# Optimization experiments

Hardware: AMD Instinct MI355X
Metric: run time of the kernel (lower is better)

Reference implementation:

```python
import jax, jax.numpy as jnp
import numpy as np
import math

IN_C = 768
CA = 384
K1 = (3, 1, 1)
K2 = (1, 3, 3)
K3 = (3, 3, 3)


def _dwconv3d(x, w, b):
    # x: [B, Ca, T, H, W]; w: [Ca, 1, kt, kh, kw]; depthwise (groups = Ca)
    pads = [(k // 2, k // 2) for k in w.shape[2:]]
    y = jax.lax.conv_general_dilated(
        x, w, window_strides=(1, 1, 1), padding=pads,
        feature_group_count=x.shape[1],
        dimension_numbers=("NCDHW", "OIDHW", "NCDHW"))
    return y + b[None, :, None, None, None]


def setup_inputs() -> dict:
    key = jax.random.key(0)
    ks = jax.random.split(key, 12)
    s = 0.02
    x = jax.random.normal(ks[0], (128, 197, IN_C), dtype=jnp.float32)
    fc1_w = jax.random.normal(ks[1], (CA, IN_C), dtype=jnp.float32) * s
    fc1_b = jnp.zeros((CA,), dtype=jnp.float32)
    conv1_w = jax.random.normal(ks[2], (CA, 1) + K1, dtype=jnp.float32) * s
    conv1_b = jax.random.normal(ks[3], (CA,), dtype=jnp.float32) * s
    conv2_w = jax.random.normal(ks[4], (CA, 1) + K2, dtype=jnp.float32) * s
    conv2_b = jax.random.normal(ks[5], (CA,), dtype=jnp.float32) * s
    conv3_w = jax.random.normal(ks[6], (CA, 1) + K3, dtype=jnp.float32) * s
    conv3_b = jax.random.normal(ks[7], (CA,), dtype=jnp.float32) * s
    proj_w = jax.random.normal(ks[8], (CA, 1) + K1, dtype=jnp.float32) * s
    proj_b = jax.random.normal(ks[9], (CA,), dtype=jnp.float32) * s
    fc2_w = jax.random.normal(ks[10], (IN_C, CA), dtype=jnp.float32) * s
    fc2_b = jnp.zeros((IN_C,), dtype=jnp.float32)
    return {
        "x": x, "fc1_w": fc1_w, "fc1_b": fc1_b,
        "conv1_w": conv1_w, "conv1_b": conv1_b,
        "conv2_w": conv2_w, "conv2_b": conv2_b,
        "conv3_w": conv3_w, "conv3_b": conv3_b,
        "proj_w": proj_w, "proj_b": proj_b,
        "fc2_w": fc2_w, "fc2_b": fc2_b,
        "T": 16,
    }


def reference(x, fc1_w, fc1_b, conv1_w, conv1_b, conv2_w, conv2_b,
              conv3_w, conv3_b, proj_w, proj_b, fc2_w, fc2_b, T):
    BT, L, C = x.shape
    B = BT // T
    H = W = round(math.sqrt(L - 1))
    Ca = fc1_w.shape[0]
    x_id = x
    # drop CLS token, project down: [BT, L-1, Ca]
    h = jnp.einsum("blc,ac->bla", x[:, 1:, :], fc1_w) + fc1_b
    # [B, Ca, T, H, W]
    h = h.reshape(B, T, H, W, Ca).transpose(0, 4, 1, 2, 3)
    identity = h
    h = (_dwconv3d(h, conv1_w, conv1_b)
         + _dwconv3d(h, conv2_w, conv2_b)
         + _dwconv3d(h, conv3_w, conv3_b)) / 3.0
    h = h + identity
    h = h + _dwconv3d(h, proj_w, proj_b)
    # back to tokens: [BT, L-1, Ca]
    h = h.transpose(0, 2, 3, 4, 1).reshape(BT, L - 1, Ca)
    h = jnp.einsum("bla,ca->blc", h, fc2_w) + fc2_b
    return x_id.at[:, 1:, :].add(h)
```

## Files before the change

### kernel.cpp

```cpp
#include <hip/hip_runtime.h>
#include <cstdint>

typedef __bf16 bf16_t;
typedef __bf16 bf16x8 __attribute__((ext_vector_type(8)));
typedef float f32x4 __attribute__((ext_vector_type(4)));

#define BT_   128
#define LTOK  197
#define CIN   768
#define CA_   384
#define TT    16
#define HH    14
#define NTOK  25088

__device__ __forceinline__ void gl_lds16(const void* g, void* l) {
  __builtin_amdgcn_global_load_lds(
      (const __attribute__((address_space(1))) unsigned int*)g,
      (__attribute__((address_space(3))) unsigned int*)l,
      16, 0, 0);
}

__global__ void prep_weights_kernel(
    const float* __restrict__ c1w, const float* __restrict__ c1b,
    const float* __restrict__ c2w, const float* __restrict__ c2b,
    const float* __restrict__ c3w, const float* __restrict__ c3b,
    const float* __restrict__ projw,
    bf16_t* __restrict__ Wtb,
    float* __restrict__ beff,
    float* __restrict__ pwt) {
  int a = blockIdx.x * blockDim.x + threadIdx.x;
  if (a >= CA_) return;
  for (int dt = 0; dt < 3; dt++)
    for (int dh = 0; dh < 3; dh++)
      for (int dw = 0; dw < 3; dw++) {
        float v = c3w[a*27 + dt*9 + dh*3 + dw];
        if (dh == 1 && dw == 1) v += c1w[a*3 + dt];
        if (dt == 1)            v += c2w[a*9 + dh*3 + dw];
        v *= (1.0f/3.0f);
        if (dt == 1 && dh == 1 && dw == 1) v += 1.0f;
        Wtb[((dt*3+dh)*3+dw)*CA_ + a] = (bf16_t)v;
      }
  beff[a] = (c1b[a] + c2b[a] + c3b[a]) * (1.0f/3.0f);
  pwt[0*CA_ + a] = projw[a*3 + 0];
  pwt[1*CA_ + a] = projw[a*3 + 1];
  pwt[2*CA_ + a] = projw[a*3 + 2];
}

__global__ void convert_w_kernel(const float* __restrict__ fc1w,
                                 const float* __restrict__ fc2w,
                                 const float* __restrict__ x,
                                 float* __restrict__ out,
                                 bf16_t* __restrict__ W1,
                                 bf16_t* __restrict__ W2) {
  int i = blockIdx.x * blockDim.x + threadIdx.x;
  if (i < CA_*CIN) { W1[i] = (bf16_t)fc1w[i]; return; }
  i -= CA_*CIN;
  if (i < CIN*CA_) { W2[i] = (bf16_t)fc2w[i]; return; }
  i -= CIN*CA_;
  if (i < BT_*CIN) {
    int bt = i / CIN, c = i % CIN;
    size_t off = (size_t)bt * LTOK * CIN + c;
    out[off] = x[off];
  }
}

__global__ __launch_bounds__(256) void gemm1_kernel(
    const float* __restrict__ x, const bf16_t* __restrict__ W1,
    const float* __restrict__ fc1b, bf16_t* __restrict__ H0) {
  __shared__ bf16_t Alds[128*32];
  __shared__ bf16_t Blds[128*32];
  const int tid  = threadIdx.x;
  const int lane = tid & 63;
  const int wave = tid >> 6;
  const int bm = blockIdx.x, bn = blockIdx.y;

  const int arow  = tid >> 1;
  const int kbase = (tid & 1) * 16;
  const int tok   = bm*128 + arow;
  const int bt    = tok / 196;
  const float* xrow = x + (size_t)(tok + bt + 1) * CIN + kbase;
  bf16_t* alds_dst = &Alds[arow*32 + kbase];

  const bf16_t* bsrc0 = W1 + (size_t)(bn*128 + (tid>>2))*CIN + (tid&3)*8;
  const bf16_t* bsrc1 = bsrc0 + (size_t)64*CIN;
  bf16_t* blds0 = &Blds[tid*8];
  bf16_t* blds1 = &Blds[(tid+256)*8];

  const int quad = lane >> 4;
  const int r16  = lane & 15;
  const int wm = (wave >> 1) * 64;
  const int wn = (wave & 1) * 64;

  f32x4 acc[4][4] = {};

  for (int k0 = 0; k0 < CIN; k0 += 32) {
    gl_lds16(bsrc0 + k0, blds0);
    gl_lds16(bsrc1 + k0, blds1);
    const float4* xp = (const float4*)(xrow + k0);
    float4 f0 = xp[0], f1 = xp[1], f2 = xp[2], f3 = xp[3];
    bf16x8 p0, p1;
    p0[0]=(bf16_t)f0.x; p0[1]=(bf16_t)f0.y; p0[2]=(bf16_t)f0.z; p0[3]=(bf16_t)f0.w;
    p0[4]=(bf16_t)f1.x; p0[5]=(bf16_t)f1.y; p0[6]=(bf16_t)f1.z; p0[7]=(bf16_t)f1.w;
    p1[0]=(bf16_t)f2.x; p1[1]=(bf16_t)f2.y; p1[2]=(bf16_t)f2.z; p1[3]=(bf16_t)f2.w;
    p1[4]=(bf16_t)f3.x; p1[5]=(bf16_t)f3.y; p1[6]=(bf16_t)f3.z; p1[7]=(bf16_t)f3.w;
    *(bf16x8*)alds_dst       = p0;
    *(bf16x8*)(alds_dst + 8) = p1;
    __syncthreads();
    bf16x8 af[4], bfr[4];
    #pragma unroll
    for (int mt = 0; mt < 4; mt++)
      af[mt] = *(const bf16x8*)&Alds[(wm + mt*16 + r16)*32 + quad*8];
    #pragma unroll
    for (int nt = 0; nt < 4; nt++)
      bfr[nt] = *(const bf16x8*)&Blds[(wn + nt*16 + r16)*32 + quad*8];
    #pragma unroll
    for (int mt = 0; mt < 4; mt++)
      #pragma unroll
      for (int nt = 0; nt < 4; nt++)
        acc[mt][nt] = __builtin_amdgcn_mfma_f32_16x16x32_bf16(af[mt], bfr[nt], acc[mt][nt], 0, 0, 0);
    __syncthreads();
  }

  #pragma unroll
  for (int nt = 0; nt < 4; nt++) {
    const int col = bn*128 + wn + nt*16 + r16;
    const float bias = fc1b[col];
    #pragma unroll
    for (int mt = 0; mt < 4; mt++) {
      const int row0 = bm*128 + wm + mt*16 + quad*4;
      #pragma unroll
      for (int rg = 0; rg < 4; rg++)
        H0[(size_t)(row0 + rg)*CA_ + col] = (bf16_t)(acc[mt][nt][rg] + bias);
    }
  }
}

__global__ __launch_bounds__(192) void conv_kernel(
    const bf16_t* __restrict__ H0,
    const bf16_t* __restrict__ Wtb,
    const float* __restrict__ beff,
    const float* __restrict__ pwt,
    const float* __restrict__ pb,
    bf16_t* __restrict__ Z) {
  __shared__ bf16_t Wlds[27*CA_];
  __shared__ float  ybuf[2][2][CA_];

  const int tid = threadIdx.x;
  {
    const uint4* src = (const uint4*)Wtb;
    uint4* dst = (uint4*)Wlds;
    #pragma unroll
    for (int i = 0; i < 7; i++) {
      int idx = tid + i*192;
      if (idx < 27*CA_/8) dst[idx] = src[idx];
    }
  }

  const int blk  = blockIdx.x;
  const int b    = blk & 7;
  const int pair = blk >> 3;
  const int cg   = tid % 48;
  const int ct   = tid / 48;
  const int col  = ct >> 1;
  const int th   = ct & 1;
  const int hw   = pair*2 + col;
  const int h    = hw / HH, w = hw % HH;
  const int c0   = cg * 8;
  const int t0   = th * 8;

  float y[8][8];
  {
    f32x4 bv0 = *(const f32x4*)(beff + c0);
    f32x4 bv1 = *(const f32x4*)(beff + c0 + 4);
    #pragma unroll
    for (int i = 0; i < 8; i++) {
      #pragma unroll
      for (int c = 0; c < 4; c++) { y[i][c] = bv0[c]; y[i][c+4] = bv1[c]; }
    }
  }

  __syncthreads();

  const size_t rowstride = (size_t)196*CA_;
  const bf16_t* base_t0 = H0 + ((size_t)(b*TT + t0)*196)*CA_ + c0;
  const int tau_e_off = th ? -1 : 8;

  for (int j = 0; j < 9; j++) {
    const int dh = j / 3, dw = j - dh*3;
    const int h2 = h + dh - 1, w2 = w + dw - 1;
    const bool ok = ((unsigned)h2 < HH) && ((unsigned)w2 < HH);
    const int sp = ok ? (h2*HH + w2) : hw;
    const float m = ok ? 1.0f : 0.0f;

    const bf16x8 wv0 = *(const bf16x8*)&Wlds[(0*9+j)*CA_ + c0];
    const bf16x8 wv1 = *(const bf16x8*)&Wlds[(1*9+j)*CA_ + c0];
    const bf16x8 wv2 = *(const bf16x8*)&Wlds[(2*9+j)*CA_ + c0];
    float mw0[8], mw1[8], mw2[8];
    #pragma unroll
    for (int c = 0; c < 8; c++) {
      mw0[c] = m * (float)wv0[c];
      mw1[c] = m * (float)wv1[c];
      mw2[c] = m * (float)wv2[c];
    }

    const bf16_t* tp = base_t0 + (size_t)sp*CA_;
    bf16x8 gv[8];
    #pragma unroll
    for (int i = 0; i < 8; i++)
      gv[i] = *(const bf16x8*)(tp + (ptrdiff_t)i*(ptrdiff_t)rowstride);
    const bf16x8 ge = *(const bf16x8*)(tp + (ptrdiff_t)tau_e_off*(ptrdiff_t)rowstride);

    #pragma unroll
    for (int i = 0; i < 8; i++) {
      float gf[8];
      #pragma unroll
      for (int c = 0; c < 8; c++) gf[c] = (float)gv[i][c];
      #pragma unroll
      for (int c = 0; c < 8; c++) y[i][c] += gf[c]*mw1[c];
      if (i > 0) {
        #pragma unroll
        for (int c = 0; c < 8; c++) y[i-1][c] += gf[c]*mw2[c];
      }
      if (i < 7) {
        #pragma unroll
        for (int c = 0; c < 8; c++) y[i+1][c] += gf[c]*mw0[c];
      }
    }
    {
      float gf[8];
      #pragma unroll
      for (int c = 0; c < 8; c++) gf[c] = (float)ge[c];
      if (th) {
        #pragma unroll
        for (int c = 0; c < 8; c++) y[0][c] += gf[c]*mw0[c];
      } else {
        #pragma unroll
        for (int c = 0; c < 8; c++) y[7][c] += gf[c]*mw2[c];
      }
    }
  }

  #pragma unroll
  for (int c = 0; c < 8; c++) ybuf[col][th][c0+c] = th ? y[0][c] : y[7][c];
  __syncthreads();
  float yedge[8];
  #pragma unroll
  for (int c = 0; c < 8; c++) yedge[c] = ybuf[col][1-th][c0+c];

  float p0[8], p1[8], p2[8], pbv[8];
  {
    f32x4 a0 = *(const f32x4*)(pwt + 0*CA_ + c0), a1 = *(const f32x4*)(pwt + 0*CA_ + c0 + 4);
    f32x4 b0 = *(const f32x4*)(pwt + 1*CA_ + c0), b1 = *(const f32x4*)(pwt + 1*CA_ + c0 + 4);
    f32x4 d0 = *(const f32x4*)(pwt + 2*CA_ + c0), d1 = *(const f32x4*)(pwt + 2*CA_ + c0 + 4);
    f32x4 e0 = *(const f32x4*)(pb + c0),          e1 = *(const f32x4*)(pb + c0 + 4);
    #pragma unroll
    for (int c = 0; c < 4; c++) {
      p0[c]=a0[c]; p0[c+4]=a1[c];
      p1[c]=b0[c]; p1[c+4]=b1[c];
      p2[c]=d0[c]; p2[c+4]=d1[c];
      pbv[c]=e0[c]; pbv[c+4]=e1[c];
    }
  }

  bf16_t* zbase = Z + ((size_t)(b*TT + t0)*196 + hw)*CA_ + c0;
  #pragma unroll
  for (int i = 0; i < 8; i++) {
    bf16x8 zo;
    #pragma unroll
    for (int c = 0; c < 8; c++) {
      const float ym = (i > 0) ? y[i-1][c] : (th ? yedge[c] : 0.f);
      const float yp = (i < 7) ? y[i+1][c] : (th ? 0.f : yedge[c]);
      const float z  = y[i][c] + pbv[c] + p0[c]*ym + p1[c]*y[i][c] + p2[c]*yp;
      zo[c] = (bf16_t)z;
    }
    *(bf16x8*)(zbase + (size_t)i*rowstride) = zo;
  }
}

__global__ __launch_bounds__(256) void gemm2_kernel(
    const bf16_t* __restrict__ Z, const bf16_t* __restrict__ W2,
    const float* __restrict__ fc2b, const float* __restrict__ x,
    float* __restrict__ out) {
  __shared__ bf16_t Alds[128*32];
  __shared__ bf16_t Blds[128*32];
  const int tid  = threadIdx.x;
  const int lane = tid & 63;
  const int wave = tid >> 6;
  const int bm = blockIdx.x, bn = blockIdx.y;

  const bf16_t* asrc0 = Z  + (size_t)(bm*128 + (tid>>2))*CA_ + (tid&3)*8;
  const bf16_t* asrc1 = asrc0 + (size_t)64*CA_;
  const bf16_t* bsrc0 = W2 + (size_t)(bn*128 + (tid>>2))*CA_ + (tid&3)*8;
  const bf16_t* bsrc1 = bsrc0 + (size_t)64*CA_;
  bf16_t* alds0 = &Alds[tid*8];
  bf16_t* alds1 = &Alds[(tid+256)*8];
  bf16_t* blds0 = &Blds[tid*8];
  bf16_t* blds1 = &Blds[(tid+256)*8];

  const int quad = lane >> 4;
  const int r16  = lane & 15;
  const int wm = (wave >> 1) * 64;
  const int wn = (wave & 1) * 64;

  f32x4 acc[4][4] = {};

  for (int k0 = 0; k0 < CA_; k0 += 32) {
    gl_lds16(asrc0 + k0, alds0);
    gl_lds16(asrc1 + k0, alds1);
    gl_lds16(bsrc0 + k0, blds0);
    gl_lds16(bsrc1 + k0, blds1);
    __syncthreads();
    bf16x8 af[4], bfr[4];
    #pragma unroll
    for (int mt = 0; mt < 4; mt++)
      af[mt] = *(const bf16x8*)&Alds[(wm + mt*16 + r16)*32 + quad*8];
    #pragma unroll
    for (int nt = 0; nt < 4; nt++)
      bfr[nt] = *(const bf16x8*)&Blds[(wn + nt*16 + r16)*32 + quad*8];
    #pragma unroll
    for (int mt = 0; mt < 4; mt++)
      #pragma unroll
      for (int nt = 0; nt < 4; nt++)
        acc[mt][nt] = __builtin_amdgcn_mfma_f32_16x16x32_bf16(af[mt], bfr[nt], acc[mt][nt], 0, 0, 0);
    __syncthreads();
  }

  #pragma unroll
  for (int nt = 0; nt < 4; nt++) {
    const int col = bn*128 + wn + nt*16 + r16;
    const float bias = fc2b[col];
    #pragma unroll
    for (int mt = 0; mt < 4; mt++) {
      #pragma unroll
      for (int rg = 0; rg < 4; rg++) {
        const int tok = bm*128 + wm + mt*16 + quad*4 + rg;
        const int bt  = tok / 196;
        const size_t o = (size_t)(tok + bt + 1)*CIN + col;
        out[o] = x[o] + acc[mt][nt][rg] + bias;
      }
    }
  }
}

extern "C" void kernel_launch(void* const* d_in, const int* in_sizes, int n_in,
                              void* d_out, int out_size, void* d_ws, size_t ws_size,
                              hipStream_t stream) {
  (void)in_sizes; (void)n_in; (void)out_size; (void)ws_size;
  const float* x    = (const float*)d_in[0];
  const float* fc1w = (const float*)d_in[1];
  const float* fc1b = (const float*)d_in[2];
  const float* c1w  = (const float*)d_in[3];
  const float* c1b  = (const float*)d_in[4];
  const float* c2w  = (const float*)d_in[5];
  const float* c2b  = (const float*)d_in[6];
  const float* c3w  = (const float*)d_in[7];
  const float* c3b  = (const float*)d_in[8];
  const float* pw   = (const float*)d_in[9];
  const float* pb   = (const float*)d_in[10];
  const float* fc2w = (const float*)d_in[11];
  const float* fc2b = (const float*)d_in[12];
  float* out = (float*)d_out;

  char* ws = (char*)d_ws;
  bf16_t* W1   = (bf16_t*)(ws);
  bf16_t* W2   = (bf16_t*)(ws + 589824);
  bf16_t* Wtb  = (bf16_t*)(ws + 1179648);
  float*  beff = (float*) (ws + 1200384);
  float*  pwt  = (float*) (ws + 1201920);
  bf16_t* H0   = (bf16_t*)(ws + 1206528);
  bf16_t* Z    = (bf16_t*)(ws + 20474112);

  prep_weights_kernel<<<dim3(2), dim3(192), 0, stream>>>(
      c1w, c1b, c2w, c2b, c3w, c3b, pw, Wtb, beff, pwt);
  convert_w_kernel<<<dim3(2688), dim3(256), 0, stream>>>(fc1w, fc2w, x, out, W1, W2);
  gemm1_kernel<<<dim3(196, 3), dim3(256), 0, stream>>>(x, W1, fc1b, H0);
  conv_kernel<<<dim3(784), dim3(192), 0, stream>>>(H0, Wtb, beff, pwt, pb, Z);
  gemm2_kernel<<<dim3(196, 6), dim3(256), 0, stream>>>(Z, W2, fc2b, x, out);
}
```

Measured before the change: 262.1 us.

## Double-buffer LDS tiles in both GEMM kernels to overlap loads with MFMA

```diff
diff --git a/kernel.cpp b/kernel.cpp
--- a/kernel.cpp
+++ b/kernel.cpp
@@ -67,8 +67,8 @@
 __global__ __launch_bounds__(256) void gemm1_kernel(
     const float* __restrict__ x, const bf16_t* __restrict__ W1,
     const float* __restrict__ fc1b, bf16_t* __restrict__ H0) {
-  __shared__ bf16_t Alds[128*32];
-  __shared__ bf16_t Blds[128*32];
+  __shared__ bf16_t Alds[2][128*32];
+  __shared__ bf16_t Blds[2][128*32];
   const int tid  = threadIdx.x;
   const int lane = tid & 63;
   const int wave = tid >> 6;
@@ -79,12 +79,12 @@
   const int tok   = bm*128 + arow;
   const int bt    = tok / 196;
   const float* xrow = x + (size_t)(tok + bt + 1) * CIN + kbase;
-  bf16_t* alds_dst = &Alds[arow*32 + kbase];
+  const int aoff = arow*32 + kbase;
 
   const bf16_t* bsrc0 = W1 + (size_t)(bn*128 + (tid>>2))*CIN + (tid&3)*8;
   const bf16_t* bsrc1 = bsrc0 + (size_t)64*CIN;
-  bf16_t* blds0 = &Blds[tid*8];
-  bf16_t* blds1 = &Blds[(tid+256)*8];
+  const int boff0 = tid*8;
+  const int boff1 = (tid+256)*8;
 
   const int quad = lane >> 4;
   const int r16  = lane & 15;
@@ -93,32 +93,57 @@
 
   f32x4 acc[4][4] = {};
 
-  for (int k0 = 0; k0 < CIN; k0 += 32) {
-    gl_lds16(bsrc0 + k0, blds0);
-    gl_lds16(bsrc1 + k0, blds1);
-    const float4* xp = (const float4*)(xrow + k0);
+  {
+    const float4* xp = (const float4*)xrow;
     float4 f0 = xp[0], f1 = xp[1], f2 = xp[2], f3 = xp[3];
+    gl_lds16(bsrc0, &Blds[0][boff0]);
+    gl_lds16(bsrc1, &Blds[0][boff1]);
     bf16x8 p0, p1;
     p0[0]=(bf16_t)f0.x; p0[1]=(bf16_t)f0.y; p0[2]=(bf16_t)f0.z; p0[3]=(bf16_t)f0.w;
     p0[4]=(bf16_t)f1.x; p0[5]=(bf16_t)f1.y; p0[6]=(bf16_t)f1.z; p0[7]=(bf16_t)f1.w;
     p1[0]=(bf16_t)f2.x; p1[1]=(bf16_t)f2.y; p1[2]=(bf16_t)f2.z; p1[3]=(bf16_t)f2.w;
     p1[4]=(bf16_t)f3.x; p1[5]=(bf16_t)f3.y; p1[6]=(bf16_t)f3.z; p1[7]=(bf16_t)f3.w;
-    *(bf16x8*)alds_dst       = p0;
-    *(bf16x8*)(alds_dst + 8) = p1;
-    __syncthreads();
+    *(bf16x8*)&Alds[0][aoff]     = p0;
+    *(bf16x8*)&Alds[0][aoff + 8] = p1;
+  }
+  __syncthreads();
+
+  int cur = 0;
+  for (int k0 = 0; k0 < CIN; k0 += 32) {
+    const int kn = k0 + 32;
+    const bool more = (kn < CIN);
+    float4 f0, f1, f2, f3;
+    if (more) {
+      const float4* xp = (const float4*)(xrow + kn);
+      f0 = xp[0]; f1 = xp[1]; f2 = xp[2]; f3 = xp[3];
+      gl_lds16(bsrc0 + kn, &Blds[cur^1][boff0]);
+      gl_lds16(bsrc1 + kn, &Blds[cur^1][boff1]);
+    }
+
     bf16x8 af[4], bfr[4];
     #pragma unroll
     for (int mt = 0; mt < 4; mt++)
-      af[mt] = *(const bf16x8*)&Alds[(wm + mt*16 + r16)*32 + quad*8];
+      af[mt] = *(const bf16x8*)&Alds[cur][(wm + mt*16 + r16)*32 + quad*8];
     #pragma unroll
     for (int nt = 0; nt < 4; nt++)
-      bfr[nt] = *(const bf16x8*)&Blds[(wn + nt*16 + r16)*32 + quad*8];
+      bfr[nt] = *(const bf16x8*)&Blds[cur][(wn + nt*16 + r16)*32 + quad*8];
     #pragma unroll
     for (int mt = 0; mt < 4; mt++)
       #pragma unroll
       for (int nt = 0; nt < 4; nt++)
         acc[mt][nt] = __builtin_amdgcn_mfma_f32_16x16x32_bf16(af[mt], bfr[nt], acc[mt][nt], 0, 0, 0);
+
+    if (more) {
+      bf16x8 p0, p1;
+      p0[0]=(bf16_t)f0.x; p0[1]=(bf16_t)f0.y; p0[2]=(bf16_t)f0.z; p0[3]=(bf16_t)f0.w;
+      p0[4]=(bf16_t)f1.x; p0[5]=(bf16_t)f1.y; p0[6]=(bf16_t)f1.z; p0[7]=(bf16_t)f1.w;
+      p1[0]=(bf16_t)f2.x; p1[1]=(bf16_t)f2.y; p1[2]=(bf16_t)f2.z; p1[3]=(bf16_t)f2.w;
+      p1[4]=(bf16_t)f3.x; p1[5]=(bf16_t)f3.y; p1[6]=(bf16_t)f3.z; p1[7]=(bf16_t)f3.w;
+      *(bf16x8*)&Alds[cur^1][aoff]     = p0;
+      *(bf16x8*)&Alds[cur^1][aoff + 8] = p1;
+    }
     __syncthreads();
+    cur ^= 1;
   }
 
   #pragma unroll
@@ -281,8 +306,8 @@
     const bf16_t* __restrict__ Z, const bf16_t* __restrict__ W2,
     const float* __restrict__ fc2b, const float* __restrict__ x,
     float* __restrict__ out) {
-  __shared__ bf16_t Alds[128*32];
-  __shared__ bf16_t Blds[128*32];
+  __shared__ bf16_t Alds[2][128*32];
+  __shared__ bf16_t Blds[2][128*32];
   const int tid  = threadIdx.x;
   const int lane = tid & 63;
   const int wave = tid >> 6;
@@ -292,10 +317,8 @@
   const bf16_t* asrc1 = asrc0 + (size_t)64*CA_;
   const bf16_t* bsrc0 = W2 + (size_t)(bn*128 + (tid>>2))*CA_ + (tid&3)*8;
   const bf16_t* bsrc1 = bsrc0 + (size_t)64*CA_;
-  bf16_t* alds0 = &Alds[tid*8];
-  bf16_t* alds1 = &Alds[(tid+256)*8];
-  bf16_t* blds0 = &Blds[tid*8];
-  bf16_t* blds1 = &Blds[(tid+256)*8];
+  const int aoff0 = tid*8;
+  const int aoff1 = (tid+256)*8;
 
   const int quad = lane >> 4;
   const int r16  = lane & 15;
@@ -304,25 +327,35 @@
 
   f32x4 acc[4][4] = {};
 
+  gl_lds16(asrc0, &Alds[0][aoff0]);
+  gl_lds16(asrc1, &Alds[0][aoff1]);
+  gl_lds16(bsrc0, &Blds[0][aoff0]);
+  gl_lds16(bsrc1, &Blds[0][aoff1]);
+  __syncthreads();
+
+  int cur = 0;
   for (int k0 = 0; k0 < CA_; k0 += 32) {
-    gl_lds16(asrc0 + k0, alds0);
-    gl_lds16(asrc1 + k0, alds1);
-    gl_lds16(bsrc0 + k0, blds0);
-    gl_lds16(bsrc1 + k0, blds1);
-    __syncthreads();
+    const int kn = k0 + 32;
+    if (kn < CA_) {
+      gl_lds16(asrc0 + kn, &Alds[cur^1][aoff0]);
+      gl_lds16(asrc1 + kn, &Alds[cur^1][aoff1]);
+      gl_lds16(bsrc0 + kn, &Blds[cur^1][aoff0]);
+      gl_lds16(bsrc1 + kn, &Blds[cur^1][aoff1]);
+    }
     bf16x8 af[4], bfr[4];
     #pragma unroll
     for (int mt = 0; mt < 4; mt++)
-      af[mt] = *(const bf16x8*)&Alds[(wm + mt*16 + r16)*32 + quad*8];
+      af[mt] = *(const bf16x8*)&Alds[cur][(wm + mt*16 + r16)*32 + quad*8];
     #pragma unroll
     for (int nt = 0; nt < 4; nt++)
-      bfr[nt] = *(const bf16x8*)&Blds[(wn + nt*16 + r16)*32 + quad*8];
+      bfr[nt] = *(const bf16x8*)&Blds[cur][(wn + nt*16 + r16)*32 + quad*8];
     #pragma unroll
     for (int mt = 0; mt < 4; mt++)
       #pragma unroll
       for (int nt = 0; nt < 4; nt++)
         acc[mt][nt] = __builtin_amdgcn_mfma_f32_16x16x32_bf16(af[mt], bfr[nt], acc[mt][nt], 0, 0, 0);
     __syncthreads();
+    cur ^= 1;
   }
 
   #pragma unroll
```

Result: no change. 262.4 us (+0.1%).

## Triple-buffer LDS pipelines in both GEMMs with 64x192 tiles

Applied to the files above, without the earlier changes.

```diff
diff --git a/kernel.cpp b/kernel.cpp
--- a/kernel.cpp
+++ b/kernel.cpp
@@ -19,6 +19,10 @@
       (__attribute__((address_space(3))) unsigned int*)l,
       16, 0, 0);
 }
+
+#define SBAR() do { __builtin_amdgcn_sched_barrier(0); \
+                    __builtin_amdgcn_s_barrier(); \
+                    __builtin_amdgcn_sched_barrier(0); } while (0)
 
 __global__ void prep_weights_kernel(
     const float* __restrict__ c1w, const float* __restrict__ c1b,
@@ -67,72 +71,103 @@
 __global__ __launch_bounds__(256) void gemm1_kernel(
     const float* __restrict__ x, const bf16_t* __restrict__ W1,
     const float* __restrict__ fc1b, bf16_t* __restrict__ H0) {
-  __shared__ bf16_t Alds[128*32];
-  __shared__ bf16_t Blds[128*32];
+  __shared__ bf16_t Alds[3][2048];
+  __shared__ bf16_t Blds[3][6144];
   const int tid  = threadIdx.x;
   const int lane = tid & 63;
   const int wave = tid >> 6;
   const int bm = blockIdx.x, bn = blockIdx.y;
 
-  const int arow  = tid >> 1;
-  const int kbase = (tid & 1) * 16;
-  const int tok   = bm*128 + arow;
-  const int bt    = tok / 196;
-  const float* xrow = x + (size_t)(tok + bt + 1) * CIN + kbase;
-  bf16_t* alds_dst = &Alds[arow*32 + kbase];
-
-  const bf16_t* bsrc0 = W1 + (size_t)(bn*128 + (tid>>2))*CIN + (tid&3)*8;
-  const bf16_t* bsrc1 = bsrc0 + (size_t)64*CIN;
-  bf16_t* blds0 = &Blds[tid*8];
-  bf16_t* blds1 = &Blds[(tid+256)*8];
+  const int arow = tid >> 2;
+  const int tok  = bm*64 + arow;
+  const int bt   = tok / 196;
+  const float* xsrc = x + (size_t)(tok + bt + 1)*CIN + (tid & 3)*8;
+  const bf16_t* bsrc = W1 + (size_t)(bn*192 + arow)*CIN + (tid & 3)*8;
 
   const int quad = lane >> 4;
   const int r16  = lane & 15;
-  const int wm = (wave >> 1) * 64;
-  const int wn = (wave & 1) * 64;
-
-  f32x4 acc[4][4] = {};
-
-  for (int k0 = 0; k0 < CIN; k0 += 32) {
-    gl_lds16(bsrc0 + k0, blds0);
-    gl_lds16(bsrc1 + k0, blds1);
-    const float4* xp = (const float4*)(xrow + k0);
-    float4 f0 = xp[0], f1 = xp[1], f2 = xp[2], f3 = xp[3];
-    bf16x8 p0, p1;
-    p0[0]=(bf16_t)f0.x; p0[1]=(bf16_t)f0.y; p0[2]=(bf16_t)f0.z; p0[3]=(bf16_t)f0.w;
-    p0[4]=(bf16_t)f1.x; p0[5]=(bf16_t)f1.y; p0[6]=(bf16_t)f1.z; p0[7]=(bf16_t)f1.w;
-    p1[0]=(bf16_t)f2.x; p1[1]=(bf16_t)f2.y; p1[2]=(bf16_t)f2.z; p1[3]=(bf16_t)f2.w;
-    p1[4]=(bf16_t)f3.x; p1[5]=(bf16_t)f3.y; p1[6]=(bf16_t)f3.z; p1[7]=(bf16_t)f3.w;
-    *(bf16x8*)alds_dst       = p0;
-    *(bf16x8*)(alds_dst + 8) = p1;
-    __syncthreads();
-    bf16x8 af[4], bfr[4];
-    #pragma unroll
-    for (int mt = 0; mt < 4; mt++)
-      af[mt] = *(const bf16x8*)&Alds[(wm + mt*16 + r16)*32 + quad*8];
-    #pragma unroll
-    for (int nt = 0; nt < 4; nt++)
-      bfr[nt] = *(const bf16x8*)&Blds[(wn + nt*16 + r16)*32 + quad*8];
-    #pragma unroll
-    for (int mt = 0; mt < 4; mt++)
-      #pragma unroll
-      for (int nt = 0; nt < 4; nt++)
-        acc[mt][nt] = __builtin_amdgcn_mfma_f32_16x16x32_bf16(af[mt], bfr[nt], acc[mt][nt], 0, 0, 0);
-    __syncthreads();
-  }
+  const int wn   = wave * 48;
+
+  f32x4 acc[4][3] = {};
+  float4 fa, fb;
+  float4 ca, cb;
+
+#define G1_LDF(K) do { const float4* xp_ = (const float4*)(xsrc + (K)); \
+                       fa = xp_[0]; fb = xp_[1]; } while (0)
+#define G1_GLB(B, K) do { const bf16_t* s_ = bsrc + (K); \
+    bf16_t* d_ = &Blds[B][0] + tid*8; \
+    gl_lds16(s_,                   d_); \
+    gl_lds16(s_ +  64*(size_t)CIN, d_ + 2048); \
+    gl_lds16(s_ + 128*(size_t)CIN, d_ + 4096); } while (0)
+#define G1_CVT(B) do { bf16x8 p_; \
+    p_[0]=(bf16_t)ca.x; p_[1]=(bf16_t)ca.y; p_[2]=(bf16_t)ca.z; p_[3]=(bf16_t)ca.w; \
+    p_[4]=(bf16_t)cb.x; p_[5]=(bf16_t)cb.y; p_[6]=(bf16_t)cb.z; p_[7]=(bf16_t)cb.w; \
+    *(bf16x8*)(&Alds[B][0] + tid*8) = p_; \
+    ca = fa; cb = fb; } while (0)
+#define G1_MMA(B) do { bf16x8 af_[4], bf_[3]; \
+    _Pragma("unroll") \
+    for (int mt = 0; mt < 4; mt++) \
+      af_[mt] = *(const bf16x8*)(&Alds[B][0] + (mt*16 + r16)*32 + quad*8); \
+    _Pragma("unroll") \
+    for (int nt = 0; nt < 3; nt++) \
+      bf_[nt] = *(const bf16x8*)(&Blds[B][0] + (wn + nt*16 + r16)*32 + quad*8); \
+    _Pragma("unroll") \
+    for (int mt = 0; mt < 4; mt++) \
+      _Pragma("unroll") \
+      for (int nt = 0; nt < 3; nt++) \
+        acc[mt][nt] = __builtin_amdgcn_mfma_f32_16x16x32_bf16(af_[mt], bf_[nt], acc[mt][nt], 0, 0, 0); \
+  } while (0)
+
+  { const float4* xp_ = (const float4*)xsrc; ca = xp_[0]; cb = xp_[1]; }
+  G1_GLB(0, 0);
+  G1_LDF(32);
+  G1_GLB(1, 32);
+  G1_CVT(0);
+  asm volatile("s_waitcnt vmcnt(5) lgkmcnt(0)" ::: "memory");
+  SBAR();
+
+  #pragma unroll 1
+  for (int ii = 0; ii < 7; ii++) {
+    #pragma unroll
+    for (int j = 0; j < 3; j++) {
+      const int i  = ii*3 + j;
+      const int kc = i*32;
+      G1_LDF(kc + 64);
+      G1_GLB((j + 2) % 3, kc + 64);
+      G1_MMA(j);
+      G1_CVT((j + 1) % 3);
+      asm volatile("s_waitcnt vmcnt(5) lgkmcnt(0)" ::: "memory");
+      SBAR();
+    }
+  }
+  G1_LDF(23*32);
+  G1_GLB(2, 23*32);
+  G1_MMA(0);
+  G1_CVT(1);
+  asm volatile("s_waitcnt vmcnt(5) lgkmcnt(0)" ::: "memory");
+  SBAR();
+  G1_MMA(1);
+  G1_CVT(2);
+  asm volatile("s_waitcnt vmcnt(0) lgkmcnt(0)" ::: "memory");
+  SBAR();
+  G1_MMA(2);
 
   #pragma unroll
-  for (int nt = 0; nt < 4; nt++) {
-    const int col = bn*128 + wn + nt*16 + r16;
+  for (int nt = 0; nt < 3; nt++) {
+    const int col = bn*192 + wn + nt*16 + r16;
     const float bias = fc1b[col];
     #pragma unroll
     for (int mt = 0; mt < 4; mt++) {
-      const int row0 = bm*128 + wm + mt*16 + quad*4;
+      const int row0 = bm*64 + mt*16 + quad*4;
       #pragma unroll
       for (int rg = 0; rg < 4; rg++)
         H0[(size_t)(row0 + rg)*CA_ + col] = (bf16_t)(acc[mt][nt][rg] + bias);
     }
   }
+#undef G1_LDF
+#undef G1_GLB
+#undef G1_CVT
+#undef G1_MMA
 }
 
 __global__ __launch_bounds__(192) void conv_kernel(
@@ -281,65 +316,86 @@
     const bf16_t* __restrict__ Z, const bf16_t* __restrict__ W2,
     const float* __restrict__ fc2b, const float* __restrict__ x,
     float* __restrict__ out) {
-  __shared__ bf16_t Alds[128*32];
-  __shared__ bf16_t Blds[128*32];
+  __shared__ bf16_t Alds[3][2048];
+  __shared__ bf16_t Blds[3][6144];
   const int tid  = threadIdx.x;
   const int lane = tid & 63;
   const int wave = tid >> 6;
   const int bm = blockIdx.x, bn = blockIdx.y;
 
-  const bf16_t* asrc0 = Z  + (size_t)(bm*128 + (tid>>2))*CA_ + (tid&3)*8;
-  const bf16_t* asrc1 = asrc0 + (size_t)64*CA_;
-  const bf16_t* bsrc0 = W2 + (size_t)(bn*128 + (tid>>2))*CA_ + (tid&3)*8;
-  const bf16_t* bsrc1 = bsrc0 + (size_t)64*CA_;
-  bf16_t* alds0 = &Alds[tid*8];
-  bf16_t* alds1 = &Alds[(tid+256)*8];
-  bf16_t* blds0 = &Blds[tid*8];
-  bf16_t* blds1 = &Blds[(tid+256)*8];
+  const int arow = tid >> 2;
+  const bf16_t* asrc = Z  + (size_t)(bm*64  + arow)*CA_ + (tid & 3)*8;
+  const bf16_t* bsrc = W2 + (size_t)(bn*192 + arow)*CA_ + (tid & 3)*8;
 
   const int quad = lane >> 4;
   const int r16  = lane & 15;
-  const int wm = (wave >> 1) * 64;
-  const int wn = (wave & 1) * 64;
-
-  f32x4 acc[4][4] = {};
-
-  for (int k0 = 0; k0 < CA_; k0 += 32) {
-    gl_lds16(asrc0 + k0, alds0);
-    gl_lds16(asrc1 + k0, alds1);
-    gl_lds16(bsrc0 + k0, blds0);
-    gl_lds16(bsrc1 + k0, blds1);
-    __syncthreads();
-    bf16x8 af[4], bfr[4];
-    #pragma unroll
-    for (int mt = 0; mt < 4; mt++)
-      af[mt] = *(const bf16x8*)&Alds[(wm + mt*16 + r16)*32 + quad*8];
-    #pragma unroll
-    for (int nt = 0; nt < 4; nt++)
-      bfr[nt] = *(const bf16x8*)&Blds[(wn + nt*16 + r16)*32 + quad*8];
-    #pragma unroll
-    for (int mt = 0; mt < 4; mt++)
-      #pragma unroll
-      for (int nt = 0; nt < 4; nt++)
-        acc[mt][nt] = __builtin_amdgcn_mfma_f32_16x16x32_bf16(af[mt], bfr[nt], acc[mt][nt], 0, 0, 0);
-    __syncthreads();
-  }
+  const int wn   = wave * 48;
+
+  f32x4 acc[4][3] = {};
+
+#define G2_GL(B, K) do { \
+    gl_lds16(asrc + (K), &Alds[B][0] + tid*8); \
+    const bf16_t* s_ = bsrc + (K); \
+    bf16_t* d_ = &Blds[B][0] + tid*8; \
+    gl_lds16(s_,                   d_); \
+    gl_lds16(s_ +  64*(size_t)CA_, d_ + 2048); \
+    gl_lds16(s_ + 128*(size_t)CA_, d_ + 4096); } while (0)
+#define G2_MMA(B) do { bf16x8 af_[4], bf_[3]; \
+    _Pragma("unroll") \
+    for (int mt = 0; mt < 4; mt++) \
+      af_[mt] = *(const bf16x8*)(&Alds[B][0] + (mt*16 + r16)*32 + quad*8); \
+    _Pragma("unroll") \
+    for (int nt = 0; nt < 3; nt++) \
+      bf_[nt] = *(const bf16x8*)(&Blds[B][0] + (wn + nt*16 + r16)*32 + quad*8); \
+    _Pragma("unroll") \
+    for (int mt = 0; mt < 4; mt++) \
+      _Pragma("unroll") \
+      for (int nt = 0; nt < 3; nt++) \
+        acc[mt][nt] = __builtin_amdgcn_mfma_f32_16x16x32_bf16(af_[mt], bf_[nt], acc[mt][nt], 0, 0, 0); \
+  } while (0)
+
+  G2_GL(0, 0);
+  G2_GL(1, 32);
+  asm volatile("s_waitcnt vmcnt(4)" ::: "memory");
+  SBAR();
+
+  #pragma unroll 1
+  for (int ii = 0; ii < 3; ii++) {
+    #pragma unroll
+    for (int j = 0; j < 3; j++) {
+      const int i = ii*3 + j;
+      G2_GL((j + 2) % 3, i*32 + 64);
+      G2_MMA(j);
+      asm volatile("s_waitcnt vmcnt(4)" ::: "memory");
+      SBAR();
+    }
+  }
+  G2_GL(2, 11*32);
+  G2_MMA(0);
+  asm volatile("s_waitcnt vmcnt(4)" ::: "memory");
+  SBAR();
+  G2_MMA(1);
+  asm volatile("s_waitcnt vmcnt(0)" ::: "memory");
+  SBAR();
+  G2_MMA(2);
 
   #pragma unroll
-  for (int nt = 0; nt < 4; nt++) {
-    const int col = bn*128 + wn + nt*16 + r16;
+  for (int nt = 0; nt < 3; nt++) {
+    const int col = bn*192 + wn + nt*16 + r16;
     const float bias = fc2b[col];
     #pragma unroll
     for (int mt = 0; mt < 4; mt++) {
       #pragma unroll
       for (int rg = 0; rg < 4; rg++) {
-        const int tok = bm*128 + wm + mt*16 + quad*4 + rg;
+        const int tok = bm*64 + mt*16 + quad*4 + rg;
         const int bt  = tok / 196;
         const size_t o = (size_t)(tok + bt + 1)*CIN + col;
         out[o] = x[o] + acc[mt][nt][rg] + bias;
       }
     }
   }
+#undef G2_GL
+#undef G2_MMA
 }
 
 extern "C" void kernel_launch(void* const* d_in, const int* in_sizes, int n_in,
@@ -373,7 +429,7 @@
   prep_weights_kernel<<<dim3(2), dim3(192), 0, stream>>>(
       c1w, c1b, c2w, c2b, c3w, c3b, pw, Wtb, beff, pwt);
   convert_w_kernel<<<dim3(2688), dim3(256), 0, stream>>>(fc1w, fc2w, x, out, W1, W2);
-  gemm1_kernel<<<dim3(196, 3), dim3(256), 0, stream>>>(x, W1, fc1b, H0);
+  gemm1_kernel<<<dim3(392, 2), dim3(256), 0, stream>>>(x, W1, fc1b, H0);
   conv_kernel<<<dim3(784), dim3(192), 0, stream>>>(H0, Wtb, beff, pwt, pb, Z);
-  gemm2_kernel<<<dim3(196, 6), dim3(256), 0, stream>>>(Z, W2, fc2b, x, out);
-}
+  gemm2_kernel<<<dim3(392, 4), dim3(256), 0, stream>>>(Z, W2, fc2b, x, out);
+}
```

Result: slower. 283.2 us (+8.1%).

## Pre-swizzle GEMM weights into MFMA fragment layout and drop LDS staging

Applied to the files above, without the earlier changes.

```diff
diff --git a/kernel.cpp b/kernel.cpp
--- a/kernel.cpp
+++ b/kernel.cpp
@@ -12,13 +12,6 @@
 #define TT    16
 #define HH    14
 #define NTOK  25088
-
-__device__ __forceinline__ void gl_lds16(const void* g, void* l) {
-  __builtin_amdgcn_global_load_lds(
-      (const __attribute__((address_space(1))) unsigned int*)g,
-      (__attribute__((address_space(3))) unsigned int*)l,
-      16, 0, 0);
-}
 
 __global__ void prep_weights_kernel(
     const float* __restrict__ c1w, const float* __restrict__ c1b,
@@ -50,12 +43,26 @@
                                  const float* __restrict__ fc2w,
                                  const float* __restrict__ x,
                                  float* __restrict__ out,
-                                 bf16_t* __restrict__ W1,
-                                 bf16_t* __restrict__ W2) {
+                                 bf16_t* __restrict__ W1f,
+                                 bf16_t* __restrict__ W2f) {
   int i = blockIdx.x * blockDim.x + threadIdx.x;
-  if (i < CA_*CIN) { W1[i] = (bf16_t)fc1w[i]; return; }
+  if (i < CA_*CIN) {
+    int f = i >> 9, t = i & 511, l = t >> 3, j = t & 7;
+    int ch = f / 24, cb = f % 24;
+    int col = cb*16 + (l & 15);
+    int k   = ch*32 + (l >> 4)*8 + j;
+    W1f[i] = (bf16_t)fc1w[col*CIN + k];
+    return;
+  }
   i -= CA_*CIN;
-  if (i < CIN*CA_) { W2[i] = (bf16_t)fc2w[i]; return; }
+  if (i < CIN*CA_) {
+    int f = i >> 9, t = i & 511, l = t >> 3, j = t & 7;
+    int ch = f / 48, cb = f % 48;
+    int col = cb*16 + (l & 15);
+    int k   = ch*32 + (l >> 4)*8 + j;
+    W2f[i] = (bf16_t)fc2w[col*CA_ + k];
+    return;
+  }
   i -= CIN*CA_;
   if (i < BT_*CIN) {
     int bt = i / CIN, c = i % CIN;
@@ -64,70 +71,53 @@
   }
 }
 
-__global__ __launch_bounds__(256) void gemm1_kernel(
-    const float* __restrict__ x, const bf16_t* __restrict__ W1,
+__global__ __launch_bounds__(64) void gemm1_kernel(
+    const float* __restrict__ x, const bf16_t* __restrict__ W1f,
     const float* __restrict__ fc1b, bf16_t* __restrict__ H0) {
-  __shared__ bf16_t Alds[128*32];
-  __shared__ bf16_t Blds[128*32];
-  const int tid  = threadIdx.x;
-  const int lane = tid & 63;
-  const int wave = tid >> 6;
-  const int bm = blockIdx.x, bn = blockIdx.y;
-
-  const int arow  = tid >> 1;
-  const int kbase = (tid & 1) * 16;
-  const int tok   = bm*128 + arow;
-  const int bt    = tok / 196;
-  const float* xrow = x + (size_t)(tok + bt + 1) * CIN + kbase;
-  bf16_t* alds_dst = &Alds[arow*32 + kbase];
-
-  const bf16_t* bsrc0 = W1 + (size_t)(bn*128 + (tid>>2))*CIN + (tid&3)*8;
-  const bf16_t* bsrc1 = bsrc0 + (size_t)64*CIN;
-  bf16_t* blds0 = &Blds[tid*8];
-  bf16_t* blds1 = &Blds[(tid+256)*8];
-
-  const int quad = lane >> 4;
-  const int r16  = lane & 15;
-  const int wm = (wave >> 1) * 64;
-  const int wn = (wave & 1) * 64;
-
-  f32x4 acc[4][4] = {};
-
-  for (int k0 = 0; k0 < CIN; k0 += 32) {
-    gl_lds16(bsrc0 + k0, blds0);
-    gl_lds16(bsrc1 + k0, blds1);
-    const float4* xp = (const float4*)(xrow + k0);
-    float4 f0 = xp[0], f1 = xp[1], f2 = xp[2], f3 = xp[3];
-    bf16x8 p0, p1;
-    p0[0]=(bf16_t)f0.x; p0[1]=(bf16_t)f0.y; p0[2]=(bf16_t)f0.z; p0[3]=(bf16_t)f0.w;
-    p0[4]=(bf16_t)f1.x; p0[5]=(bf16_t)f1.y; p0[6]=(bf16_t)f1.z; p0[7]=(bf16_t)f1.w;
-    p1[0]=(bf16_t)f2.x; p1[1]=(bf16_t)f2.y; p1[2]=(bf16_t)f2.z; p1[3]=(bf16_t)f2.w;
-    p1[4]=(bf16_t)f3.x; p1[5]=(bf16_t)f3.y; p1[6]=(bf16_t)f3.z; p1[7]=(bf16_t)f3.w;
-    *(bf16x8*)alds_dst       = p0;
-    *(bf16x8*)(alds_dst + 8) = p1;
-    __syncthreads();
-    bf16x8 af[4], bfr[4];
+  const int lane = threadIdx.x;
+  const int wg = blockIdx.x;
+  const int bm = blockIdx.y;
+  const int quad = lane >> 4, r16 = lane & 15;
+  const int wn = wg * 96;
+
+  const float* xa[4];
+  #pragma unroll
+  for (int mt = 0; mt < 4; mt++) {
+    int tok = bm*64 + mt*16 + r16;
+    int bt = tok / 196;
+    xa[mt] = x + (size_t)(tok + bt + 1)*CIN + quad*8;
+  }
+  const bf16_t* wb = W1f + (size_t)(wg*6)*512 + lane*8;
+
+  f32x4 acc[4][6] = {};
+  #pragma unroll
+  for (int i = 0; i < 24; i++) {
+    bf16x8 bfr[6];
+    #pragma unroll
+    for (int nt = 0; nt < 6; nt++)
+      bfr[nt] = *(const bf16x8*)(wb + (size_t)(i*24 + nt)*512);
+    bf16x8 af[4];
+    #pragma unroll
+    for (int mt = 0; mt < 4; mt++) {
+      const float4* p = (const float4*)(xa[mt] + i*32);
+      float4 u = p[0], v = p[1];
+      af[mt][0]=(bf16_t)u.x; af[mt][1]=(bf16_t)u.y; af[mt][2]=(bf16_t)u.z; af[mt][3]=(bf16_t)u.w;
+      af[mt][4]=(bf16_t)v.x; af[mt][5]=(bf16_t)v.y; af[mt][6]=(bf16_t)v.z; af[mt][7]=(bf16_t)v.w;
+    }
     #pragma unroll
     for (int mt = 0; mt < 4; mt++)
-      af[mt] = *(const bf16x8*)&Alds[(wm + mt*16 + r16)*32 + quad*8];
-    #pragma unroll
-    for (int nt = 0; nt < 4; nt++)
-      bfr[nt] = *(const bf16x8*)&Blds[(wn + nt*16 + r16)*32 + quad*8];
-    #pragma unroll
-    for (int mt = 0; mt < 4; mt++)
-      #pragma unroll
-      for (int nt = 0; nt < 4; nt++)
+      #pragma unroll
+      for (int nt = 0; nt < 6; nt++)
         acc[mt][nt] = __builtin_amdgcn_mfma_f32_16x16x32_bf16(af[mt], bfr[nt], acc[mt][nt], 0, 0, 0);
-    __syncthreads();
-  }
-
-  #pragma unroll
-  for (int nt = 0; nt < 4; nt++) {
-    const int col = bn*128 + wn + nt*16 + r16;
+  }
+
+  #pragma unroll
+  for (int nt = 0; nt < 6; nt++) {
+    const int col = wn + nt*16 + r16;
     const float bias = fc1b[col];
     #pragma unroll
     for (int mt = 0; mt < 4; mt++) {
-      const int row0 = bm*128 + wm + mt*16 + quad*4;
+      const int row0 = bm*64 + mt*16 + quad*4;
       #pragma unroll
       for (int rg = 0; rg < 4; rg++)
         H0[(size_t)(row0 + rg)*CA_ + col] = (bf16_t)(acc[mt][nt][rg] + bias);
@@ -277,66 +267,54 @@
   }
 }
 
-__global__ __launch_bounds__(256) void gemm2_kernel(
-    const bf16_t* __restrict__ Z, const bf16_t* __restrict__ W2,
+__global__ __launch_bounds__(64) void gemm2_kernel(
+    const bf16_t* __restrict__ Z, const bf16_t* __restrict__ W2f,
     const float* __restrict__ fc2b, const float* __restrict__ x,
     float* __restrict__ out) {
-  __shared__ bf16_t Alds[128*32];
-  __shared__ bf16_t Blds[128*32];
-  const int tid  = threadIdx.x;
-  const int lane = tid & 63;
-  const int wave = tid >> 6;
-  const int bm = blockIdx.x, bn = blockIdx.y;
-
-  const bf16_t* asrc0 = Z  + (size_t)(bm*128 + (tid>>2))*CA_ + (tid&3)*8;
-  const bf16_t* asrc1 = asrc0 + (size_t)64*CA_;
-  const bf16_t* bsrc0 = W2 + (size_t)(bn*128 + (tid>>2))*CA_ + (tid&3)*8;
-  const bf16_t* bsrc1 = bsrc0 + (size_t)64*CA_;
-  bf16_t* alds0 = &Alds[tid*8];
-  bf16_t* alds1 = &Alds[(tid+256)*8];
-  bf16_t* blds0 = &Blds[tid*8];
-  bf16_t* blds1 = &Blds[(tid+256)*8];
-
-  const int quad = lane >> 4;
-  const int r16  = lane & 15;
-  const int wm = (wave >> 1) * 64;
-  const int wn = (wave & 1) * 64;
-
-  f32x4 acc[4][4] = {};
-
-  for (int k0 = 0; k0 < CA_; k0 += 32) {
-    gl_lds16(asrc0 + k0, alds0);
-    gl_lds16(asrc1 + k0, alds1);
-    gl_lds16(bsrc0 + k0, blds0);
-    gl_lds16(bsrc1 + k0, blds1);
-    __syncthreads();
-    bf16x8 af[4], bfr[4];
+  const int lane = threadIdx.x;
+  const int wg = blockIdx.x;
+  const int bm = blockIdx.y;
+  const int quad = lane >> 4, r16 = lane & 15;
+  const int wn = wg * 96;
+
+  const bf16_t* za[4];
+  #pragma unroll
+  for (int mt = 0; mt < 4; mt++) {
+    int tok = bm*64 + mt*16 + r16;
+    za[mt] = Z + (size_t)tok*CA_ + quad*8;
+  }
+  const bf16_t* wb = W2f + (size_t)(wg*6)*512 + lane*8;
+
+  f32x4 acc[4][6] = {};
+  #pragma unroll
+  for (int i = 0; i < 12; i++) {
+    bf16x8 bfr[6];
+    #pragma unroll
+    for (int nt = 0; nt < 6; nt++)
+      bfr[nt] = *(const bf16x8*)(wb + (size_t)(i*48 + nt)*512);
+    bf16x8 af[4];
     #pragma unroll
     for (int mt = 0; mt < 4; mt++)
-      af[mt] = *(const bf16x8*)&Alds[(wm + mt*16 + r16)*32 + quad*8];
-    #pragma unroll
-    for (int nt = 0; nt < 4; nt++)
-      bfr[nt] = *(const bf16x8*)&Blds[(wn + nt*16 + r16)*32 + quad*8];
+      af[mt] = *(const bf16x8*)(za[mt] + i*32);
     #pragma unroll
     for (int mt = 0; mt < 4; mt++)
       #pragma unroll
-      for (int nt = 0; nt < 4; nt++)
+      for (int nt = 0; nt < 6; nt++)
         acc[mt][nt] = __builtin_amdgcn_mfma_f32_16x16x32_bf16(af[mt], bfr[nt], acc[mt][nt], 0, 0, 0);
-    __syncthreads();
-  }
-
-  #pragma unroll
-  for (int nt = 0; nt < 4; nt++) {
-    const int col = bn*128 + wn + nt*16 + r16;
-    const float bias = fc2b[col];
-    #pragma unroll
-    for (int mt = 0; mt < 4; mt++) {
-      #pragma unroll
-      for (int rg = 0; rg < 4; rg++) {
-        const int tok = bm*128 + wm + mt*16 + quad*4 + rg;
-        const int bt  = tok / 196;
-        const size_t o = (size_t)(tok + bt + 1)*CIN + col;
-        out[o] = x[o] + acc[mt][nt][rg] + bias;
+  }
+
+  #pragma unroll
+  for (int mt = 0; mt < 4; mt++) {
+    #pragma unroll
+    for (int rg = 0; rg < 4; rg++) {
+      const int tok = bm*64 + mt*16 + quad*4 + rg;
+      const int bt = tok / 196;
+      const size_t rowo = (size_t)(tok + bt + 1)*CIN;
+      #pragma unroll
+      for (int nt = 0; nt < 6; nt++) {
+        const int col = wn + nt*16 + r16;
+        const size_t o = rowo + col;
+        out[o] = x[o] + acc[mt][nt][rg] + fc2b[col];
       }
     }
   }
@@ -362,18 +340,18 @@
   float* out = (float*)d_out;
 
   char* ws = (char*)d_ws;
-  bf16_t* W1   = (bf16_t*)(ws);
-  bf16_t* W2   = (bf16_t*)(ws + 589824);
-  bf16_t* Wtb  = (bf16_t*)(ws + 1179648);
-  float*  beff = (float*) (ws + 1200384);
-  float*  pwt  = (float*) (ws + 1201920);
-  bf16_t* H0   = (bf16_t*)(ws + 1206528);
-  bf16_t* Z    = (bf16_t*)(ws + 20474112);
+  bf16_t* W2f  = (bf16_t*)(ws);
+  bf16_t* Wtb  = (bf16_t*)(ws + 589824);
+  float*  beff = (float*) (ws + 610560);
+  float*  pwt  = (float*) (ws + 612096);
+  bf16_t* H0   = (bf16_t*)(ws + 616704);
+  bf16_t* Z    = (bf16_t*)(ws + 19884288);
+  bf16_t* W1f  = (bf16_t*)(ws + 19884288);
 
   prep_weights_kernel<<<dim3(2), dim3(192), 0, stream>>>(
       c1w, c1b, c2w, c2b, c3w, c3b, pw, Wtb, beff, pwt);
-  convert_w_kernel<<<dim3(2688), dim3(256), 0, stream>>>(fc1w, fc2w, x, out, W1, W2);
-  gemm1_kernel<<<dim3(196, 3), dim3(256), 0, stream>>>(x, W1, fc1b, H0);
+  convert_w_kernel<<<dim3(2688), dim3(256), 0, stream>>>(fc1w, fc2w, x, out, W1f, W2f);
+  gemm1_kernel<<<dim3(4, 392), dim3(64), 0, stream>>>(x, W1f, fc1b, H0);
   conv_kernel<<<dim3(784), dim3(192), 0, stream>>>(H0, Wtb, beff, pwt, pb, Z);
-  gemm2_kernel<<<dim3(196, 6), dim3(256), 0, stream>>>(Z, W2, fc2b, x, out);
-}
+  gemm2_kernel<<<dim3(8, 392), dim3(64), 0, stream>>>(Z, W2f, fc2b, x, out);
+}
```

After: 325.9 us. 1.24x slower.
